# Kernel tuning notes

Hardware: AMD Instinct MI355X
Metric: run time of the kernel (lower is better)

The kernel has to match this reference:

```python
import jax, jax.numpy as jnp
import numpy as np

V_REST = 0.0
V_RESET = 0.0
V_TH = 1.27
TAU = 50.0
SPIKE_DURATION = 1
SCALE = 100.0  # SurrGradSpike.scale


@jax.custom_vjp
def spike(x):
    return (x > 0).astype(x.dtype)

def _spike_fwd(x):
    return (x > 0).astype(x.dtype), x

def _spike_bwd(x, g):
    # normalized negative part of fast sigmoid (Zenke & Ganguli 2018)
    return (g / (SCALE * jnp.abs(x) + 1.0) ** 2,)

spike.defvjp(_spike_fwd, _spike_bwd)


def _shift(a, k):
    # a[:, j] -> a[:, j + k], zero padded out of range
    if k == 0:
        return a
    if k > 0:
        return jnp.pad(a[:, k:], ((0, 0), (0, k)))
    return jnp.pad(a[:, :k], ((0, 0), (-k, 0)))


def _lif(ode, decay):
    ode2 = ode[..., 0]          # [B, T]
    B, T = ode2.shape
    ode_t = ode2.T              # [T, B] for scan

    def step(carry, inp):
        v, counter, z = carry   # z = remaining steps whose dv reads are zeroed
        t, x = inp
        v = v - decay * (v - V_REST)
        v = jnp.where(counter == 1, V_RESET, v)
        # dv[:, t] was zeroed by a spike within the previous 5 steps (torch in-place window)
        x_eff = jnp.where(z > 0, 0.0, x)
        v = v + x_eff
        v = jnp.where(counter > 1, V_TH, v)
        s = spike(v - V_TH)
        s_d = jax.lax.stop_gradient(s)
        counter = counter + (SPIKE_DURATION + 1) * s_d
        v = jnp.where(counter > 1, V_TH, v)
        # spike at t zeroes dv[:, t-1:t+6]; at t==0 the torch slice [-1:6] is empty
        z = jnp.where((s_d > 0) & (t >= 1), 5.0, jnp.maximum(z - 1.0, 0.0))
        counter = jnp.maximum(counter - 1.0, 0.0)
        return (v, counter, z), (v, s, s_d)

    v0 = jnp.full((B,), V_REST, dtype=ode2.dtype)
    c0 = jnp.zeros((B,), dtype=ode2.dtype)
    z0 = jnp.zeros((B,), dtype=ode2.dtype)
    ts = jnp.arange(T)
    _, (v_rec, s_rec, sd_rec) = jax.lax.scan(step, (v0, c0, z0), (ts, ode_t))
    v_rec = v_rec.T             # [B, T]
    s_rec = s_rec.T             # [B, T]

    sp = sd_rec.T > 0           # detached spike mask [B, T]
    sp = sp.at[:, 0].set(False)  # spike at t=0 zeroes nothing (empty slice in torch)
    # column j of dv is zeroed iff a spike occurred at t' in [j-5, j+1]
    zero_mask = jnp.zeros_like(sp)
    for k in range(-5, 2):
        zero_mask = zero_mask | _shift(sp, k)
    dv = jnp.where(zero_mask, 0.0, ode2)
    return v_rec, s_rec, dv


def setup_inputs() -> dict:
    key = jax.random.key(0)
    B, T = 2048, 4096
    ode = jax.random.normal(key, (B, T, 1), dtype=jnp.float32)
    decay = jnp.float32(1.0 / TAU)  # LIF.decay parameter (learn_tau=False)
    return {"ode": ode, "decay": decay}


def reference(ode, decay):
    return _lif(ode, decay)
```

## Files before the change

### kernel.cpp

```cpp
#include <hip/hip_runtime.h>

constexpr int   T   = 4096;
constexpr float VTH = 1.27f;
constexpr int   K   = 64;
constexpr int   L   = T / K;
constexpr int   LG  = L / 4;
constexpr int   WGG = 160;

__device__ __forceinline__ bool sstep(float x, float decay, float& v, unsigned& h, bool& gate) {
    float t1 = __fmul_rn(decay, v);
    float vd = __fsub_rn(v, t1);
    float xe = gate ? 0.0f : x;
    float vn = __fadd_rn(vd, xe);
    bool  s  = vn > VTH;
    v = s ? 0.0f : vn;
    bool g4 = (h & 15u) != 0u;
    h = (h << 1) | (s ? 1u : 0u);
    gate = s || g4;
    return s;
}

__device__ __forceinline__ bool ostep(float x, float decay, float& v, unsigned& h, bool& gate,
                                      float& vo, float& so, float& dvo, float xprev) {
    float t1 = __fmul_rn(decay, v);
    float vd = __fsub_rn(v, t1);
    float xe = gate ? 0.0f : x;
    float vn = __fadd_rn(vd, xe);
    bool  s  = vn > VTH;
    vo = s ? VTH  : vn;
    so = s ? 1.0f : 0.0f;
    v  = s ? 0.0f : vn;
    bool z6 = s || ((h & 63u) != 0u);
    dvo = z6 ? 0.0f : xprev;
    bool g4 = (h & 15u) != 0u;
    h = (h << 1) | (s ? 1u : 0u);
    gate = s || g4;
    return s;
}

__device__ __forceinline__ void ogroup(float4 X, float decay, float& v, unsigned& h, bool& gate,
                                       float& xprev, float4& vo, float4& so,
                                       float& close, float& px, float& py, float& pz) {
    ostep(X.x, decay, v, h, gate, vo.x, so.x, close, xprev); xprev = X.x;
    ostep(X.y, decay, v, h, gate, vo.y, so.y, px,    xprev); xprev = X.y;
    ostep(X.z, decay, v, h, gate, vo.z, so.z, py,    xprev); xprev = X.z;
    ostep(X.w, decay, v, h, gate, vo.w, so.w, pz,    xprev); xprev = X.w;
}

#define WVM(N) do { asm volatile("s_waitcnt vmcnt(" #N ")" ::: "memory"); \
                    __builtin_amdgcn_sched_barrier(0); } while (0)
#define WLG()  do { asm volatile("s_waitcnt lgkmcnt(0)" ::: "memory"); \
                    __builtin_amdgcn_sched_barrier(0); } while (0)

using GU32 = const __attribute__((address_space(1))) unsigned int;
using LU32 = __attribute__((address_space(3))) unsigned int;

__device__ __forceinline__ void stage8(const float* src0, float4* lbuf) {
    LU32* lp = (LU32*)lbuf;
#pragma unroll
    for (int j = 0; j < 8; ++j)
        __builtin_amdgcn_global_load_lds((GU32*)(src0 + (size_t)j * 8 * T),
                                         lp + j * 256, 16, 0, 0);
}

__global__ __launch_bounds__(64, 2)
void lif_spec(const float* __restrict__ ode, const float* __restrict__ decay_p,
              float* __restrict__ vout, float* __restrict__ sout, float* __restrict__ dvout,
              float2* __restrict__ Sst, float2* __restrict__ Est, int B) {
    __shared__ float4 xin[64 * 8];
    __shared__ float4 stg[64 * 8];

    const int tid = threadIdx.x;
    const int gg  = blockIdx.x * 64;
    const int rb  = gg % B;
    const int k   = gg / B;
    const int b   = rb + tid;
    const float decay = decay_p[0];
    const int t7 = tid & 7, t3 = tid >> 3;
    const int sw = t7 ^ t3;

    const int g0f = k * LG;
    const int wgg = (k == 0) ? 0 : (g0f < WGG ? g0f : WGG);
    const int nw  = wgg >> 3;
    const int gstart = g0f - wgg;

    float v = 0.0f; unsigned h = 0u; bool gate = false;
    float xprev = 0.0f;

    float xla = (k < K - 1) ? ode[(size_t)b * T + (size_t)(k + 1) * L] : 0.0f;

#define STAGE(t) stage8(ode + ((size_t)(rb + t3) * T \
                               + (size_t)(gstart + 8 * (t)) * 4 + sw * 4), xin)
    float4 G0, G1, G2, G3, G4, G5, G6, G7;
#define RD8() do { G0 = xin[tid*8 + (0^t7)]; G1 = xin[tid*8 + (1^t7)]; \
                   G2 = xin[tid*8 + (2^t7)]; G3 = xin[tid*8 + (3^t7)]; \
                   G4 = xin[tid*8 + (4^t7)]; G5 = xin[tid*8 + (5^t7)]; \
                   G6 = xin[tid*8 + (6^t7)]; G7 = xin[tid*8 + (7^t7)]; } while (0)
#define WG4(G) { sstep(G.x, decay, v, h, gate); sstep(G.y, decay, v, h, gate); \
                 sstep(G.z, decay, v, h, gate); sstep(G.w, decay, v, h, gate); }

    STAGE(0);

    if (nw > 0) {
        const bool t0row = (gstart == 0);
        for (int t = 0; t < nw; ++t) {
            WVM(0);
            RD8();
            WLG();
            STAGE(t + 1);
            if (t == 0 && t0row) {
                sstep(G0.x, decay, v, h, gate); h = 0u; gate = false;
                sstep(G0.y, decay, v, h, gate);
                sstep(G0.z, decay, v, h, gate);
                sstep(G0.w, decay, v, h, gate);
            } else { WG4(G0) }
            WG4(G1) WG4(G2) WG4(G3) WG4(G4) WG4(G5) WG4(G6) WG4(G7)
        }
    }

    float4 VA0, VA1, VA2, VA3, VA4, VA5, VA6, VA7;
    float4 SA0, SA1, SA2, SA3, SA4, SA5, SA6, SA7;
    float4 DA0, DA1, DA2, DA3, DA4, DA5, DA6, DA7;
    float4 DB0, DB1, DB2, DB3, DB4, DB5, DB6, DB7;
    float dumm;

#define OGR(X, Vd, Sd, CloseL, Dd) { \
        ostep(X.x, decay, v, h, gate, Vd.x, Sd.x, CloseL, xprev); xprev = X.x; \
        ostep(X.y, decay, v, h, gate, Vd.y, Sd.y, Dd.x,   xprev); xprev = X.y; \
        ostep(X.z, decay, v, h, gate, Vd.z, Sd.z, Dd.y,   xprev); xprev = X.z; \
        ostep(X.w, decay, v, h, gate, Vd.w, Sd.w, Dd.z,   xprev); xprev = X.w; }

#define FL(R0,R1,R2,R3,R4,R5,R6,R7, dst, poff) { \
        stg[tid*8 + (0^t7)] = R0; stg[tid*8 + (1^t7)] = R1; \
        stg[tid*8 + (2^t7)] = R2; stg[tid*8 + (3^t7)] = R3; \
        stg[tid*8 + (4^t7)] = R4; stg[tid*8 + (5^t7)] = R5; \
        stg[tid*8 + (6^t7)] = R6; stg[tid*8 + (7^t7)] = R7; \
        WLG(); \
        _Pragma("unroll") \
        for (int jj = 0; jj < 8; ++jj) { \
            int rr = jj * 8 + t3; \
            size_t off = (size_t)(rb + rr) * T + (size_t)k * L + (poff) * 32 + t7 * 4; \
            *(float4*)((dst) + off) = stg[rr * 8 + sw]; \
        } \
        WLG(); }

    {
        WVM(0);
        RD8();
        WLG();
        if (nw > 0) Sst[k * B + b] = make_float2(v, __uint_as_float(h & 127u));
        STAGE(nw + 1);
        if (k == 0) {
            bool s0 = ostep(G0.x, decay, v, h, gate, VA0.x, SA0.x, dumm, xprev); xprev = G0.x;
            h = 0u; gate = false;
            bool s1 = ostep(G0.y, decay, v, h, gate, VA0.y, SA0.y, DA0.x, xprev); xprev = G0.y;
            ostep(G0.z, decay, v, h, gate, VA0.z, SA0.z, DA0.y, xprev); xprev = G0.z;
            ostep(G0.w, decay, v, h, gate, VA0.w, SA0.w, DA0.z, xprev); xprev = G0.w;
            if (s0 && s1) VA0.z = VTH;
        } else {
            OGR(G0, VA0, SA0, dumm, DA0)
        }
        OGR(G1, VA1, SA1, DA0.w, DA1) OGR(G2, VA2, SA2, DA1.w, DA2)
        OGR(G3, VA3, SA3, DA2.w, DA3) OGR(G4, VA4, SA4, DA3.w, DA4)
        OGR(G5, VA5, SA5, DA4.w, DA5) OGR(G6, VA6, SA6, DA5.w, DA6)
        OGR(G7, VA7, SA7, DA6.w, DA7)
        FL(VA0, VA1, VA2, VA3, VA4, VA5, VA6, VA7, vout, 0)
        FL(SA0, SA1, SA2, SA3, SA4, SA5, SA6, SA7, sout, 0)
    }

    {
        WVM(16);
        RD8();
        WLG();
        OGR(G0, VA0, SA0, DA7.w, DB0)
        FL(DA0, DA1, DA2, DA3, DA4, DA5, DA6, DA7, dvout, 0)
        OGR(G1, VA1, SA1, DB0.w, DB1) OGR(G2, VA2, SA2, DB1.w, DB2)
        OGR(G3, VA3, SA3, DB2.w, DB3) OGR(G4, VA4, SA4, DB3.w, DB4)
        OGR(G5, VA5, SA5, DB4.w, DB5) OGR(G6, VA6, SA6, DB5.w, DB6)
        OGR(G7, VA7, SA7, DB6.w, DB7)
        FL(VA0, VA1, VA2, VA3, VA4, VA5, VA6, VA7, vout, 1)
        FL(SA0, SA1, SA2, SA3, SA4, SA5, SA6, SA7, sout, 1)
    }

    Est[k * B + b] = make_float2(v, __uint_as_float(h & 127u));

    if (k < K - 1) {
        float vo_, so_;
        ostep(xla, decay, v, h, gate, vo_, so_, DB7.w, xprev);
    } else {
        DB7.w = ((h & 63u) != 0u) ? 0.0f : xprev;
    }
    FL(DB0, DB1, DB2, DB3, DB4, DB5, DB6, DB7, dvout, 1)
#undef OGR
#undef FL
#undef RD8
#undef WG4
#undef STAGE
}

__global__ __launch_bounds__(64, 1)
void lif_fix(const float* __restrict__ ode, const float* __restrict__ decay_p,
             float* __restrict__ vout, float* __restrict__ sout, float* __restrict__ dvout,
             const float2* __restrict__ Sst, const float2* __restrict__ Est, int B) {
    const int b = blockIdx.x * 64 + threadIdx.x;
    const float decay = decay_p[0];

    float2 E  = Est[b];
    float2 S1 = Sst[B + b];
    float2 E1 = Est[B + b];
    for (int k = 1; k < K; ++k) {
        float2 S = S1, Ek = E1;
        if (k + 1 < K) { S1 = Sst[(k + 1) * B + b]; E1 = Est[(k + 1) * B + b]; }
        bool match = (S.x == E.x) && (__float_as_uint(S.y) == __float_as_uint(E.y));
        if (match) { E = Ek; continue; }

        const size_t bt = (size_t)b * T;
        const float4* __restrict__ x4 = (const float4*)(ode + bt);
        float4* __restrict__ v4 = (float4*)(vout + bt);
        float4* __restrict__ s4 = (float4*)(sout + bt);
        float4* __restrict__ d4 = (float4*)(dvout + bt);
        const int g0f = k * LG;

        float v = E.x; unsigned h = __float_as_uint(E.y);
        bool gate = (h & 31u) != 0u;
        float xprev = 0.0f;
        float4 pend;

        float4 Q0 = x4[g0f], Q1 = x4[g0f + 1], Q2 = x4[g0f + 2], Q3 = x4[g0f + 3];
        {
            float4 vo, so; float cl;
            ogroup(Q0, decay, v, h, gate, xprev, vo, so, cl, pend.x, pend.y, pend.z);
            v4[g0f] = vo; s4[g0f] = so;
            Q0 = x4[g0f + 4];
        }
#define FPROC(cc, Q) { float4 vo, so; float px, py, pz; \
            ogroup(Q, decay, v, h, gate, xprev, vo, so, pend.w, px, py, pz); \
            d4[g0f + (cc) - 1] = pend; \
            pend.x = px; pend.y = py; pend.z = pz; \
            v4[g0f + (cc)] = vo; s4[g0f + (cc)] = so; }
        FPROC(1, Q1) Q1 = x4[g0f + 5];
        FPROC(2, Q2) Q2 = x4[g0f + 6];
        FPROC(3, Q3) Q3 = x4[g0f + 7];
        for (int c0 = 4; c0 < LG; c0 += 4) {
            FPROC(c0,     Q0) Q0 = x4[g0f + (c0 + 4 < LG ? c0 + 4 : LG - 1)];
            FPROC(c0 + 1, Q1) Q1 = x4[g0f + (c0 + 5 < LG ? c0 + 5 : LG - 1)];
            FPROC(c0 + 2, Q2) Q2 = x4[g0f + (c0 + 6 < LG ? c0 + 6 : LG - 1)];
            FPROC(c0 + 3, Q3) Q3 = x4[g0f + (c0 + 7 < LG ? c0 + 7 : LG - 1)];
        }
#undef FPROC
        E = make_float2(v, __uint_as_float(h & 127u));
        if (k < K - 1) {
            float xla = ode[bt + (size_t)(k + 1) * L];
            float vo_, so_;
            ostep(xla, decay, v, h, gate, vo_, so_, pend.w, xprev);
        } else {
            pend.w = ((h & 63u) != 0u) ? 0.0f : xprev;
        }
        d4[g0f + LG - 1] = pend;
    }
}

extern "C" void kernel_launch(void* const* d_in, const int* in_sizes, int n_in,
                              void* d_out, int out_size, void* d_ws, size_t ws_size,
                              hipStream_t stream) {
    const float* ode   = (const float*)d_in[0];
    const float* decay = (const float*)d_in[1];
    float* out = (float*)d_out;

    const int BT = in_sizes[0];
    const int B  = BT / T;

    float* vout  = out;
    float* sout  = out + (size_t)BT;
    float* dvout = out + 2 * (size_t)BT;

    float2* Sst = (float2*)d_ws;
    float2* Est = Sst + (size_t)K * B;

    lif_spec<<<dim3((B * K) / 64), dim3(64), 0, stream>>>(ode, decay, vout, sout, dvout,
                                                          Sst, Est, B);
    lif_fix<<<dim3(B / 64), dim3(64), 0, stream>>>(ode, decay, vout, sout, dvout,
                                                   Sst, Est, B);
}
```

Before: 191.6 us.

## Halve time-chunk count, process four sub-blocks per workgroup, merge v/s store staging

```diff
diff --git a/kernel.cpp b/kernel.cpp
--- a/kernel.cpp
+++ b/kernel.cpp
@@ -2,7 +2,7 @@
 
 constexpr int   T   = 4096;
 constexpr float VTH = 1.27f;
-constexpr int   K   = 64;
+constexpr int   K   = 32;
 constexpr int   L   = T / K;
 constexpr int   LG  = L / 4;
 constexpr int   WGG = 160;
@@ -63,12 +63,13 @@
                                          lp + j * 256, 16, 0, 0);
 }
 
-__global__ __launch_bounds__(64, 2)
+__global__ __launch_bounds__(64, 1)
 void lif_spec(const float* __restrict__ ode, const float* __restrict__ decay_p,
               float* __restrict__ vout, float* __restrict__ sout, float* __restrict__ dvout,
               float2* __restrict__ Sst, float2* __restrict__ Est, int B) {
     __shared__ float4 xin[64 * 8];
-    __shared__ float4 stg[64 * 8];
+    __shared__ float4 stgA[64 * 8];
+    __shared__ float4 stgB[64 * 8];
 
     const int tid = threadIdx.x;
     const int gg  = blockIdx.x * 64;
@@ -130,17 +131,36 @@
         ostep(X.z, decay, v, h, gate, Vd.z, Sd.z, Dd.y,   xprev); xprev = X.z; \
         ostep(X.w, decay, v, h, gate, Vd.w, Sd.w, Dd.z,   xprev); xprev = X.w; }
 
-#define FL(R0,R1,R2,R3,R4,R5,R6,R7, dst, poff) { \
-        stg[tid*8 + (0^t7)] = R0; stg[tid*8 + (1^t7)] = R1; \
-        stg[tid*8 + (2^t7)] = R2; stg[tid*8 + (3^t7)] = R3; \
-        stg[tid*8 + (4^t7)] = R4; stg[tid*8 + (5^t7)] = R5; \
-        stg[tid*8 + (6^t7)] = R6; stg[tid*8 + (7^t7)] = R7; \
+#define FLVS(poff) { \
+        stgA[tid*8 + (0^t7)] = VA0; stgA[tid*8 + (1^t7)] = VA1; \
+        stgA[tid*8 + (2^t7)] = VA2; stgA[tid*8 + (3^t7)] = VA3; \
+        stgA[tid*8 + (4^t7)] = VA4; stgA[tid*8 + (5^t7)] = VA5; \
+        stgA[tid*8 + (6^t7)] = VA6; stgA[tid*8 + (7^t7)] = VA7; \
+        stgB[tid*8 + (0^t7)] = SA0; stgB[tid*8 + (1^t7)] = SA1; \
+        stgB[tid*8 + (2^t7)] = SA2; stgB[tid*8 + (3^t7)] = SA3; \
+        stgB[tid*8 + (4^t7)] = SA4; stgB[tid*8 + (5^t7)] = SA5; \
+        stgB[tid*8 + (6^t7)] = SA6; stgB[tid*8 + (7^t7)] = SA7; \
         WLG(); \
         _Pragma("unroll") \
         for (int jj = 0; jj < 8; ++jj) { \
             int rr = jj * 8 + t3; \
             size_t off = (size_t)(rb + rr) * T + (size_t)k * L + (poff) * 32 + t7 * 4; \
-            *(float4*)((dst) + off) = stg[rr * 8 + sw]; \
+            *(float4*)(vout + off) = stgA[rr * 8 + sw]; \
+            *(float4*)(sout + off) = stgB[rr * 8 + sw]; \
+        } \
+        WLG(); }
+
+#define FLDV(R0,R1,R2,R3,R4,R5,R6,R7, poff) { \
+        stgA[tid*8 + (0^t7)] = R0; stgA[tid*8 + (1^t7)] = R1; \
+        stgA[tid*8 + (2^t7)] = R2; stgA[tid*8 + (3^t7)] = R3; \
+        stgA[tid*8 + (4^t7)] = R4; stgA[tid*8 + (5^t7)] = R5; \
+        stgA[tid*8 + (6^t7)] = R6; stgA[tid*8 + (7^t7)] = R7; \
+        WLG(); \
+        _Pragma("unroll") \
+        for (int jj = 0; jj < 8; ++jj) { \
+            int rr = jj * 8 + t3; \
+            size_t off = (size_t)(rb + rr) * T + (size_t)k * L + (poff) * 32 + t7 * 4; \
+            *(float4*)(dvout + off) = stgA[rr * 8 + sw]; \
         } \
         WLG(); }
 
@@ -164,22 +184,44 @@
         OGR(G3, VA3, SA3, DA2.w, DA3) OGR(G4, VA4, SA4, DA3.w, DA4)
         OGR(G5, VA5, SA5, DA4.w, DA5) OGR(G6, VA6, SA6, DA5.w, DA6)
         OGR(G7, VA7, SA7, DA6.w, DA7)
-        FL(VA0, VA1, VA2, VA3, VA4, VA5, VA6, VA7, vout, 0)
-        FL(SA0, SA1, SA2, SA3, SA4, SA5, SA6, SA7, sout, 0)
-    }
-
+        FLVS(0)
+    }
     {
         WVM(16);
         RD8();
         WLG();
+        STAGE(nw + 2);
         OGR(G0, VA0, SA0, DA7.w, DB0)
-        FL(DA0, DA1, DA2, DA3, DA4, DA5, DA6, DA7, dvout, 0)
+        FLDV(DA0, DA1, DA2, DA3, DA4, DA5, DA6, DA7, 0)
         OGR(G1, VA1, SA1, DB0.w, DB1) OGR(G2, VA2, SA2, DB1.w, DB2)
         OGR(G3, VA3, SA3, DB2.w, DB3) OGR(G4, VA4, SA4, DB3.w, DB4)
         OGR(G5, VA5, SA5, DB4.w, DB5) OGR(G6, VA6, SA6, DB5.w, DB6)
         OGR(G7, VA7, SA7, DB6.w, DB7)
-        FL(VA0, VA1, VA2, VA3, VA4, VA5, VA6, VA7, vout, 1)
-        FL(SA0, SA1, SA2, SA3, SA4, SA5, SA6, SA7, sout, 1)
+        FLVS(1)
+    }
+    {
+        WVM(24);
+        RD8();
+        WLG();
+        STAGE(nw + 3);
+        OGR(G0, VA0, SA0, DB7.w, DA0)
+        FLDV(DB0, DB1, DB2, DB3, DB4, DB5, DB6, DB7, 1)
+        OGR(G1, VA1, SA1, DA0.w, DA1) OGR(G2, VA2, SA2, DA1.w, DA2)
+        OGR(G3, VA3, SA3, DA2.w, DA3) OGR(G4, VA4, SA4, DA3.w, DA4)
+        OGR(G5, VA5, SA5, DA4.w, DA5) OGR(G6, VA6, SA6, DA5.w, DA6)
+        OGR(G7, VA7, SA7, DA6.w, DA7)
+        FLVS(2)
+    }
+    {
+        WVM(24);
+        RD8();
+        OGR(G0, VA0, SA0, DA7.w, DB0)
+        FLDV(DA0, DA1, DA2, DA3, DA4, DA5, DA6, DA7, 2)
+        OGR(G1, VA1, SA1, DB0.w, DB1) OGR(G2, VA2, SA2, DB1.w, DB2)
+        OGR(G3, VA3, SA3, DB2.w, DB3) OGR(G4, VA4, SA4, DB3.w, DB4)
+        OGR(G5, VA5, SA5, DB4.w, DB5) OGR(G6, VA6, SA6, DB5.w, DB6)
+        OGR(G7, VA7, SA7, DB6.w, DB7)
+        FLVS(3)
     }
 
     Est[k * B + b] = make_float2(v, __uint_as_float(h & 127u));
@@ -190,9 +232,10 @@
     } else {
         DB7.w = ((h & 63u) != 0u) ? 0.0f : xprev;
     }
-    FL(DB0, DB1, DB2, DB3, DB4, DB5, DB6, DB7, dvout, 1)
+    FLDV(DB0, DB1, DB2, DB3, DB4, DB5, DB6, DB7, 3)
 #undef OGR
-#undef FL
+#undef FLVS
+#undef FLDV
 #undef RD8
 #undef WG4
 #undef STAGE
```

After: 170.4 us. 1.12x faster.
